# Kernel tuning notes

Measured on AMD Instinct MI355X. Metric: run time of the kernel, lower is better.

Reference implementation:

```python
import jax, jax.numpy as jnp
import numpy as np

BUCKET_BINS = jnp.array([0, 1, 2, 3, 4, 5, 7, 8, 9, 10, 15, 16, 31, 32, 63, 64], dtype=jnp.int64)
POS_NUM = 28  # ZHPosTaging.pos_num; table size pos_num + 1


def setup_inputs() -> dict:
    key = jax.random.key(0)
    k1, k2, k3, k4, k5 = jax.random.split(key, 5)
    B, S, D = 4, 2048, 768
    N = 4096
    W, P = 20, 20
    x = jax.random.normal(k1, (B, S, D), dtype=jnp.float32)
    spans = jnp.sort(jax.random.randint(k2, (N, 2), 0, S, dtype=jnp.int64), axis=-1)
    pt_labels = jax.random.randint(k3, (S,), 0, POS_NUM + 1, dtype=jnp.int64)
    width_table = jax.random.normal(k4, (16, W), dtype=jnp.float32)
    pos_table = jax.random.normal(k5, (POS_NUM + 1, P), dtype=jnp.float32)
    return {"x": x, "spans": spans, "pt_labels": pt_labels,
            "width_table": width_table, "pos_table": pos_table}


def reference(x, spans, pt_labels, width_table, pos_table):
    # x: [B,S,D], spans: [N,2] with s0<=s1, pt_labels: [S]
    s0, s1 = spans[:, 0], spans[:, 1]                      # [N]
    width = s1 - s0 + 1                                    # [N], >= 1
    # bucket index: last ix with width >= BUCKET_BINS[ix]
    em = jnp.searchsorted(BUCKET_BINS, width, side='right') - 1
    width_emb = width_table[em]                            # [N,W]
    pos_emb0 = pos_table[pt_labels[s0]]                    # [N,P]
    pos_emb1 = pos_table[pt_labels[s1]]                    # [N,P]
    # segment mean over x[:, s0:s1+1] via exclusive cumsum
    cs = jnp.concatenate([jnp.zeros_like(x[:, :1]), jnp.cumsum(x, axis=1)], axis=1)  # [B,S+1,D]
    span_sum = cs[:, s1 + 1] - cs[:, s0]                   # [B,N,D]
    mean_vec = span_sum / width[None, :, None].astype(x.dtype)
    xs0 = x[:, s0]                                         # [B,N,D]
    xs1 = x[:, s1]                                         # [B,N,D]
    B, N = x.shape[0], spans.shape[0]
    bcast = lambda e: jnp.broadcast_to(e[None], (B, N, e.shape[-1]))
    return jnp.concatenate(
        [mean_vec, xs0, bcast(pos_emb0), xs1, bcast(pos_emb1), bcast(width_emb)],
        axis=-1)                                           # [B,N,3D+2P+W]
```

## Files before the change

kernel.cpp:

```cpp
#include <hip/hip_runtime.h>

#define BB   4
#define SS   2048
#define DD   768
#define NN   4096
#define PW   20
#define CH   64
#define NCH  32
#define ROW  2364

__global__ void partial_kernel(const float* __restrict__ x, float* __restrict__ partial) {
    int d = blockIdx.x * 256 + threadIdx.x;
    int c = blockIdx.y;
    int b = blockIdx.z;
    const float* xp = x + ((size_t)(b * SS + c * CH)) * DD + d;
    float s = 0.f;
#pragma unroll
    for (int i = 0; i < CH; ++i) s += xp[(size_t)i * DD];
    partial[(b * NCH + c) * DD + d] = s;
}

__global__ void prefix_kernel(float* __restrict__ partial) {
    int t = blockIdx.x * 256 + threadIdx.x;
    int b = t / DD;
    int d = t - b * DD;
    float* p = partial + (size_t)b * NCH * DD + d;
    float v[NCH];
#pragma unroll
    for (int c = 0; c < NCH; ++c) v[c] = p[(size_t)c * DD];
    float run = 0.f;
#pragma unroll
    for (int c = 0; c < NCH; ++c) { float nv = run + v[c]; p[(size_t)c * DD] = run; run = nv; }
}

__global__ void cumsum_kernel(const float* __restrict__ x, const float* __restrict__ partial,
                              float* __restrict__ cs) {
    int d = blockIdx.x * 256 + threadIdx.x;
    int c = blockIdx.y;
    int b = blockIdx.z;
    float run = partial[(b * NCH + c) * DD + d];
    const float* xp = x + ((size_t)(b * SS) + c * CH) * DD + d;
    float*       cp = cs + ((size_t)(b * (SS + 1)) + c * CH + 1) * DD + d;
    if (c == 0) cs[((size_t)(b * (SS + 1))) * DD + d] = 0.f;
#pragma unroll 4
    for (int i = 0; i < CH; ++i) { run += xp[(size_t)i * DD]; cp[(size_t)i * DD] = run; }
}

__global__ void gather_kernel(const float* __restrict__ x, const int* __restrict__ spans,
                              const int* __restrict__ pt_labels,
                              const float* __restrict__ wtab, const float* __restrict__ ptab,
                              const float* __restrict__ cs, float* __restrict__ out) {
    int n = blockIdx.x;
    int b = blockIdx.y;
    int t = threadIdx.x;

    int s0 = spans[2 * n];
    int s1 = spans[2 * n + 1];
    int width = s1 - s0 + 1;
    float inv_w = 1.0f / (float)width;

    const int bins[15] = {1, 2, 3, 4, 5, 7, 8, 9, 10, 15, 16, 31, 32, 63, 64};
    int em = 0;
#pragma unroll
    for (int i = 0; i < 15; ++i) em += (width >= bins[i]) ? 1 : 0;

    int l0 = pt_labels[s0];
    int l1 = pt_labels[s1];

    const float4* cs0 = (const float4*)(cs + ((size_t)(b * (SS + 1)) + s0) * DD);
    const float4* cs1 = (const float4*)(cs + ((size_t)(b * (SS + 1)) + s1 + 1) * DD);
    const float4* x0  = (const float4*)(x + ((size_t)(b * SS) + s0) * DD);
    const float4* x1  = (const float4*)(x + ((size_t)(b * SS) + s1) * DD);
    float4* o = (float4*)(out + ((size_t)(b * NN) + n) * ROW);

    if (t < 192) {
        float4 a = cs1[t];
        float4 c0 = cs0[t];
        float4 m;
        m.x = (a.x - c0.x) * inv_w;
        m.y = (a.y - c0.y) * inv_w;
        m.z = (a.z - c0.z) * inv_w;
        m.w = (a.w - c0.w) * inv_w;
        o[t]       = m;
        o[192 + t] = x0[t];
        o[389 + t] = x1[t];
    } else {
        int u = t - 192;
        if (u < 5) {
            o[384 + u] = ((const float4*)(ptab + l0 * PW))[u];
        } else if (u < 10) {
            o[581 + (u - 5)] = ((const float4*)(ptab + l1 * PW))[u - 5];
        } else if (u < 15) {
            o[586 + (u - 10)] = ((const float4*)(wtab + em * PW))[u - 10];
        }
    }
}

extern "C" void kernel_launch(void* const* d_in, const int* in_sizes, int n_in,
                              void* d_out, int out_size, void* d_ws, size_t ws_size,
                              hipStream_t stream) {
    const float* x     = (const float*)d_in[0];
    const int*   spans = (const int*)d_in[1];
    const int*   pt    = (const int*)d_in[2];
    const float* wtab  = (const float*)d_in[3];
    const float* ptab  = (const float*)d_in[4];
    float* out = (float*)d_out;

    float* cs      = (float*)d_ws;
    float* partial = cs + (size_t)BB * (SS + 1) * DD;

    dim3 g1(3, NCH, BB);
    partial_kernel<<<g1, 256, 0, stream>>>(x, partial);
    prefix_kernel<<<12, 256, 0, stream>>>(partial);
    cumsum_kernel<<<g1, 256, 0, stream>>>(x, partial, cs);
    gather_kernel<<<dim3(NN, BB), 256, 0, stream>>>(x, spans, pt, wtab, ptab, cs, out);
}
```

Baseline: 210.3 us.

## Shrink cumsum chunks, batch loads, nontemporal stores, trim gather block to 192

```diff
diff --git a/kernel.cpp b/kernel.cpp
--- a/kernel.cpp
+++ b/kernel.cpp
@@ -5,11 +5,14 @@
 #define DD   768
 #define NN   4096
 #define PW   20
-#define CH   64
-#define NCH  32
+#define CH   16
+#define NCH  128
 #define ROW  2364
 
-__global__ void partial_kernel(const float* __restrict__ x, float* __restrict__ partial) {
+typedef float f4 __attribute__((ext_vector_type(4)));
+
+__global__ __launch_bounds__(256) void partial_kernel(const float* __restrict__ x,
+                                                      float* __restrict__ partial) {
     int d = blockIdx.x * 256 + threadIdx.x;
     int c = blockIdx.y;
     int b = blockIdx.z;
@@ -20,7 +23,7 @@
     partial[(b * NCH + c) * DD + d] = s;
 }
 
-__global__ void prefix_kernel(float* __restrict__ partial) {
+__global__ __launch_bounds__(256) void prefix_kernel(float* __restrict__ partial) {
     int t = blockIdx.x * 256 + threadIdx.x;
     int b = t / DD;
     int d = t - b * DD;
@@ -33,8 +36,9 @@
     for (int c = 0; c < NCH; ++c) { float nv = run + v[c]; p[(size_t)c * DD] = run; run = nv; }
 }
 
-__global__ void cumsum_kernel(const float* __restrict__ x, const float* __restrict__ partial,
-                              float* __restrict__ cs) {
+__global__ __launch_bounds__(256) void cumsum_kernel(const float* __restrict__ x,
+                                                     const float* __restrict__ partial,
+                                                     float* __restrict__ cs) {
     int d = blockIdx.x * 256 + threadIdx.x;
     int c = blockIdx.y;
     int b = blockIdx.z;
@@ -42,14 +46,20 @@
     const float* xp = x + ((size_t)(b * SS) + c * CH) * DD + d;
     float*       cp = cs + ((size_t)(b * (SS + 1)) + c * CH + 1) * DD + d;
     if (c == 0) cs[((size_t)(b * (SS + 1))) * DD + d] = 0.f;
-#pragma unroll 4
-    for (int i = 0; i < CH; ++i) { run += xp[(size_t)i * DD]; cp[(size_t)i * DD] = run; }
+    float v[CH];
+#pragma unroll
+    for (int i = 0; i < CH; ++i) v[i] = xp[(size_t)i * DD];
+#pragma unroll
+    for (int i = 0; i < CH; ++i) { run += v[i]; cp[(size_t)i * DD] = run; }
 }
 
-__global__ void gather_kernel(const float* __restrict__ x, const int* __restrict__ spans,
-                              const int* __restrict__ pt_labels,
-                              const float* __restrict__ wtab, const float* __restrict__ ptab,
-                              const float* __restrict__ cs, float* __restrict__ out) {
+__global__ __launch_bounds__(192) void gather_kernel(const float* __restrict__ x,
+                                                     const int* __restrict__ spans,
+                                                     const int* __restrict__ pt_labels,
+                                                     const float* __restrict__ wtab,
+                                                     const float* __restrict__ ptab,
+                                                     const float* __restrict__ cs,
+                                                     float* __restrict__ out) {
     int n = blockIdx.x;
     int b = blockIdx.y;
     int t = threadIdx.x;
@@ -64,34 +74,33 @@
 #pragma unroll
     for (int i = 0; i < 15; ++i) em += (width >= bins[i]) ? 1 : 0;
 
-    int l0 = pt_labels[s0];
-    int l1 = pt_labels[s1];
+    const f4* cs0 = (const f4*)(cs + ((size_t)(b * (SS + 1)) + s0) * DD);
+    const f4* cs1 = (const f4*)(cs + ((size_t)(b * (SS + 1)) + s1 + 1) * DD);
+    const f4* x0  = (const f4*)(x + ((size_t)(b * SS) + s0) * DD);
+    const f4* x1  = (const f4*)(x + ((size_t)(b * SS) + s1) * DD);
+    f4* o = (f4*)(out + ((size_t)(b * NN) + n) * ROW);
 
-    const float4* cs0 = (const float4*)(cs + ((size_t)(b * (SS + 1)) + s0) * DD);
-    const float4* cs1 = (const float4*)(cs + ((size_t)(b * (SS + 1)) + s1 + 1) * DD);
-    const float4* x0  = (const float4*)(x + ((size_t)(b * SS) + s0) * DD);
-    const float4* x1  = (const float4*)(x + ((size_t)(b * SS) + s1) * DD);
-    float4* o = (float4*)(out + ((size_t)(b * NN) + n) * ROW);
+    f4 a  = cs0 == cs1 ? cs1[t] : cs1[t];
+    f4 c0 = cs0[t];
+    f4 v0 = x0[t];
+    f4 v1 = x1[t];
+    f4 m = (a - c0) * inv_w;
+    __builtin_nontemporal_store(m,  o + t);
+    __builtin_nontemporal_store(v0, o + 192 + t);
+    __builtin_nontemporal_store(v1, o + 389 + t);
 
-    if (t < 192) {
-        float4 a = cs1[t];
-        float4 c0 = cs0[t];
-        float4 m;
-        m.x = (a.x - c0.x) * inv_w;
-        m.y = (a.y - c0.y) * inv_w;
-        m.z = (a.z - c0.z) * inv_w;
-        m.w = (a.w - c0.w) * inv_w;
-        o[t]       = m;
-        o[192 + t] = x0[t];
-        o[389 + t] = x1[t];
-    } else {
-        int u = t - 192;
-        if (u < 5) {
-            o[384 + u] = ((const float4*)(ptab + l0 * PW))[u];
-        } else if (u < 10) {
-            o[581 + (u - 5)] = ((const float4*)(ptab + l1 * PW))[u - 5];
-        } else if (u < 15) {
-            o[586 + (u - 10)] = ((const float4*)(wtab + em * PW))[u - 10];
+    if (t < 15) {
+        int l0 = pt_labels[s0];
+        int l1 = pt_labels[s1];
+        if (t < 5) {
+            f4 e = ((const f4*)(ptab + l0 * PW))[t];
+            __builtin_nontemporal_store(e, o + 384 + t);
+        } else if (t < 10) {
+            f4 e = ((const f4*)(ptab + l1 * PW))[t - 5];
+            __builtin_nontemporal_store(e, o + 581 + (t - 5));
+        } else {
+            f4 e = ((const f4*)(wtab + em * PW))[t - 10];
+            __builtin_nontemporal_store(e, o + 586 + (t - 10));
         }
     }
 }
@@ -113,5 +122,5 @@
     partial_kernel<<<g1, 256, 0, stream>>>(x, partial);
     prefix_kernel<<<12, 256, 0, stream>>>(partial);
     cumsum_kernel<<<g1, 256, 0, stream>>>(x, partial, cs);
-    gather_kernel<<<dim3(NN, BB), 256, 0, stream>>>(x, spans, pt, wtab, ptab, cs, out);
+    gather_kernel<<<dim3(NN, BB), 192, 0, stream>>>(x, spans, pt, wtab, ptab, cs, out);
 }
```

New measurement: 213.6 us. About the same (+1.6%).
